# Optimization experiments

Measured on AMD Instinct MI355X. Metric: run time of the kernel, lower is better.

## Reference

```python
import jax, jax.numpy as jnp
import numpy as np
from jax import lax

OUT_PC = 64   # out_channels // 4
IN_PC = 64    # in_channels // 4
KH = KW = 3
PAD = 1
STRIDE = (1, 1)


def setup_inputs() -> dict:
    key = jax.random.key(0)
    ks = jax.random.split(key, 6)
    wshape = (OUT_PC, IN_PC, KH, KW)
    fan_in = IN_PC * KH * KW
    bound_w = float(np.sqrt(6.0 / fan_in))  # ~kaiming_uniform scale
    bound_b = 1.0 / float(np.sqrt(fan_in))
    return {
        "x": jax.random.normal(ks[0], (16, IN_PC, 64, 64, 4), dtype=jnp.float32),
        "weight_r": jax.random.uniform(ks[1], wshape, jnp.float32, -bound_w, bound_w),
        "weight_i": jax.random.uniform(ks[2], wshape, jnp.float32, -bound_w, bound_w),
        "weight_j": jax.random.uniform(ks[3], wshape, jnp.float32, -bound_w, bound_w),
        "weight_k": jax.random.uniform(ks[4], wshape, jnp.float32, -bound_w, bound_w),
        "bias_r": jax.random.uniform(ks[5], (OUT_PC,), jnp.float32, -bound_b, bound_b),
    }


def _hamilton_weight(wr, wi, wj, wk):
    # Left Hamilton-product matrix: output blocks (rows) x input blocks (cols)
    # [[ r, -i, -j, -k],
    #  [ i,  r, -k,  j],
    #  [ j,  k,  r, -i],
    #  [ k, -j,  i,  r]]
    row_r = jnp.concatenate([wr, -wi, -wj, -wk], axis=1)
    row_i = jnp.concatenate([wi,  wr, -wk,  wj], axis=1)
    row_j = jnp.concatenate([wj,  wk,  wr, -wi], axis=1)
    row_k = jnp.concatenate([wk, -wj,  wi,  wr], axis=1)
    return jnp.concatenate([row_r, row_i, row_j, row_k], axis=0)  # [4*Opc, 4*Ipc, kh, kw]


def reference(x, weight_r, weight_i, weight_j, weight_k, bias_r):
    B, C, H, W, Q = x.shape  # BCHWQ, Q == 4
    # component-major channel flatten: [B, 4*C, H, W]
    x2 = jnp.transpose(x, (0, 4, 1, 2, 3)).reshape(B, Q * C, H, W)
    w_big = _hamilton_weight(weight_r, weight_i, weight_j, weight_k)
    y = lax.conv_general_dilated(
        x2, w_big, window_strides=STRIDE,
        padding=((PAD, PAD), (PAD, PAD)),
        dimension_numbers=("NCHW", "OIHW", "NCHW"))
    Ho, Wo = y.shape[2], y.shape[3]
    opc = weight_r.shape[0]
    y = y.reshape(B, 4, opc, Ho, Wo).transpose(0, 2, 3, 4, 1)  # [B, Opc, Ho, Wo, 4]
    # bias only on the real component
    bias_full = jnp.stack(
        [bias_r, jnp.zeros_like(bias_r), jnp.zeros_like(bias_r), jnp.zeros_like(bias_r)],
        axis=-1)  # [Opc, 4]
    return y + bias_full[None, :, None, None, :]
```

## Files before the change

### kernel.cpp

```cpp
#include <hip/hip_runtime.h>

typedef __attribute__((ext_vector_type(8))) short bf16x8;
typedef __attribute__((ext_vector_type(4))) float f32x4;
typedef __attribute__((ext_vector_type(16))) float f32x16;

__device__ __forceinline__ unsigned short f2bf(float f) {
  union { float f; unsigned u; } a; a.f = f;
  unsigned u = a.u;
  u += 0x7fffu + ((u >> 16) & 1u);
  return (unsigned short)(u >> 16);
}

__global__ void prep_bt(const float* __restrict__ wr, const float* __restrict__ wi,
                        const float* __restrict__ wj, const float* __restrict__ wk,
                        unsigned short* __restrict__ btg) {
  int idx = blockIdx.x * 256 + threadIdx.x;
  if (idx >= 9 * 256 * 256) return;
  int tap = idx >> 16;
  int rem = idx & 65535;
  int n = rem >> 8, k = rem & 255;
  int opc = n >> 2, qo = n & 3, c = k >> 2, qi = k & 3;
  const int   comp[4][4] = {{0,1,2,3},{1,0,3,2},{2,3,0,1},{3,2,1,0}};
  const float sgn [4][4] = {{1.f,-1.f,-1.f,-1.f},{1.f,1.f,-1.f,1.f},
                            {1.f,1.f,1.f,-1.f},{1.f,-1.f,1.f,1.f}};
  int ci = comp[qo][qi];
  const float* wp = (ci == 0) ? wr : (ci == 1) ? wi : (ci == 2) ? wj : wk;
  float v = sgn[qo][qi] * wp[(opc * 64 + c) * 9 + tap];
  btg[idx] = f2bf(v);
}

__launch_bounds__(256, 2)
__global__ void qconv_main(const float* __restrict__ x,
                           const unsigned short* __restrict__ btg,
                           const float* __restrict__ bias,
                           float* __restrict__ out) {
  __shared__ char xwin[4 * 66 * 128];

  const int tid = threadIdx.x;
  const int nb  = (blockIdx.x & 7) * 64 + (blockIdx.x >> 3);
  const int b   = nb >> 5;
  const int h0  = (nb & 31) * 2;

  const int lane = tid & 63;
  const int wn   = tid >> 6;
  const int l31  = lane & 31;
  const int l32  = lane >> 5;

  const int w_ = tid & 63;
  if (tid < 64) {
    int hh = tid >> 4, colsel = (tid >> 3) & 1, slot = tid & 7;
    int col = colsel ? 65 : 0;
    *reinterpret_cast<f32x4*>(xwin + (hh * 66 + col) * 128 + slot * 16) =
        (f32x4){0.f, 0.f, 0.f, 0.f};
  }

  f32x16 acc[2][4];
#pragma unroll
  for (int i = 0; i < 2; ++i)
#pragma unroll
    for (int j = 0; j < 4; ++j)
      acc[i][j] = (f32x16)(0.f);

  for (int ch = 0; ch < 4; ++ch) {
    __syncthreads();

#pragma unroll
    for (int i = 0; i < 16; ++i) {
      int u  = i * 256 + tid;
      int hh = (u >> 6) & 3;
      int cl = u >> 8;
      int hp = h0 + hh - 1;
      float4 v = make_float4(0.f, 0.f, 0.f, 0.f);
      if (hp >= 0 && hp < 64)
        v = *reinterpret_cast<const float4*>(
            x + (size_t)((((b * 64 + (ch * 16 + cl)) * 64 + hp) * 64 + w_) * 4));
      unsigned lo = (unsigned)f2bf(v.x) | ((unsigned)f2bf(v.y) << 16);
      unsigned hi = (unsigned)f2bf(v.z) | ((unsigned)f2bf(v.w) << 16);
      int col  = w_ + 1;
      int byte = (hh * 66 + col) * 128 + ((cl * 8) ^ ((col & 7) << 4));
      *reinterpret_cast<uint2*>(xwin + byte) = make_uint2(lo, hi);
    }
    __syncthreads();

    const unsigned short* wb =
        btg + (size_t)(wn * 64 + l31) * 256 + ch * 64 + l32 * 8;

    bf16x8 wf[2][8];
#pragma unroll
    for (int f = 0; f < 8; ++f)
      wf[0][f] = *reinterpret_cast<const bf16x8*>(
          wb + (f & 1) * 8192 + (f >> 1) * 16);

#pragma unroll
    for (int tap = 0; tap < 9; ++tap) {
      const int cur = tap & 1;
      if (tap < 8) {
#pragma unroll
        for (int f = 0; f < 8; ++f)
          wf[cur ^ 1][f] = *reinterpret_cast<const bf16x8*>(
              wb + (tap + 1) * 65536 + (f & 1) * 8192 + (f >> 1) * 16);
      }
      const int dh = tap / 3 - 1;
      const int dw = tap % 3 - 1;
#pragma unroll
      for (int kst = 0; kst < 4; ++kst) {
        bf16x8 pf[4];
#pragma unroll
        for (int fm = 0; fm < 4; ++fm) {
          int pix = fm * 32 + l31;
          int wc  = (pix & 63) + dw + 1;
          int hh  = (pix >> 6) + dh + 1;
          int off = (hh * 66 + wc) * 128 +
                    ((kst * 32 + l32 * 16) ^ ((wc & 7) << 4));
          pf[fm] = *reinterpret_cast<const bf16x8*>(xwin + off);
        }
        __builtin_amdgcn_s_setprio(1);
#pragma unroll
        for (int fn = 0; fn < 2; ++fn)
#pragma unroll
          for (int fm = 0; fm < 4; ++fm)
            acc[fn][fm] = __builtin_amdgcn_mfma_f32_32x32x16_bf16(
                wf[cur][kst * 2 + fn], pf[fm], acc[fn][fm], 0, 0, 0);
        __builtin_amdgcn_s_setprio(0);
      }
    }
  }

#pragma unroll
  for (int fn = 0; fn < 2; ++fn) {
#pragma unroll
    for (int fm = 0; fm < 4; ++fm) {
      int pix = fm * 32 + l31;
      int w   = pix & 63;
      int h   = h0 + (pix >> 6);
#pragma unroll
      for (int g = 0; g < 4; ++g) {
        int opc = wn * 16 + fn * 8 + g * 2 + l32;
        f32x4 v = {acc[fn][fm][4 * g + 0], acc[fn][fm][4 * g + 1],
                   acc[fn][fm][4 * g + 2], acc[fn][fm][4 * g + 3]};
        v.x += bias[opc];
        *reinterpret_cast<f32x4*>(
            out + (size_t)((((b * 64 + opc) * 64 + h) * 64 + w) * 4)) = v;
      }
    }
  }
}

extern "C" void kernel_launch(void* const* d_in, const int* in_sizes, int n_in,
                              void* d_out, int out_size, void* d_ws, size_t ws_size,
                              hipStream_t stream) {
  const float* x    = (const float*)d_in[0];
  const float* wr   = (const float*)d_in[1];
  const float* wi   = (const float*)d_in[2];
  const float* wj   = (const float*)d_in[3];
  const float* wk   = (const float*)d_in[4];
  const float* bias = (const float*)d_in[5];
  unsigned short* btg = (unsigned short*)d_ws;

  prep_bt<<<2304, 256, 0, stream>>>(wr, wi, wj, wk, btg);
  qconv_main<<<512, 256, 0, stream>>>(x, btg, bias, (float*)d_out);
}
```

Baseline: 114.8 us.

## Split output channels across two blocks and retile waves to 2x2 MFMA grid

Each block now computes half of the 256 output columns for a 2-row pixel tile, and the grid doubles to 1024 blocks. Waves are arranged 2x2 over rows and channel halves with smaller accumulators, which allows a launch bound of 3 blocks per SIMD group. The LDS layout changes to a k-slot-major scheme without XOR swizzle, and weights are loaded per k-step instead of being double-buffered. The trade-off is that each input window is staged and converted twice, once per channel-half block, in exchange for higher occupancy and fewer registers.

```diff
diff --git a/kernel.cpp b/kernel.cpp
--- a/kernel.cpp
+++ b/kernel.cpp
@@ -9,6 +9,9 @@
   unsigned u = a.u;
   u += 0x7fffu + ((u >> 16) & 1u);
   return (unsigned short)(u >> 16);
+}
+__device__ __forceinline__ unsigned pk(float a, float b) {
+  return (unsigned)f2bf(a) | ((unsigned)f2bf(b) << 16);
 }
 
 __global__ void prep_bt(const float* __restrict__ wr, const float* __restrict__ wi,
@@ -29,113 +32,107 @@
   btg[idx] = f2bf(v);
 }
 
-__launch_bounds__(256, 2)
+__launch_bounds__(256, 3)
 __global__ void qconv_main(const float* __restrict__ x,
                            const unsigned short* __restrict__ btg,
                            const float* __restrict__ bias,
                            float* __restrict__ out) {
-  __shared__ char xwin[4 * 66 * 128];
+  __shared__ char xwin[4 * 8 * 66 * 16];
 
   const int tid = threadIdx.x;
-  const int nb  = (blockIdx.x & 7) * 64 + (blockIdx.x >> 3);
-  const int b   = nb >> 5;
-  const int h0  = (nb & 31) * 2;
+  const int nb  = (blockIdx.x & 7) * 128 + (blockIdx.x >> 3);
+  const int mt  = nb >> 1;
+  const int nt  = nb & 1;
+  const int b   = mt >> 5;
+  const int h0  = (mt & 31) * 2;
 
   const int lane = tid & 63;
-  const int wn   = tid >> 6;
+  const int wid  = tid >> 6;
+  const int wm   = wid & 1;
+  const int wnh  = wid >> 1;
   const int l31  = lane & 31;
   const int l32  = lane >> 5;
 
-  const int w_ = tid & 63;
+  const int w_ = lane;
+  const int sh = wid;
+
   if (tid < 64) {
-    int hh = tid >> 4, colsel = (tid >> 3) & 1, slot = tid & 7;
-    int col = colsel ? 65 : 0;
-    *reinterpret_cast<f32x4*>(xwin + (hh * 66 + col) * 128 + slot * 16) =
+    int hh = tid >> 4, ks = (tid >> 1) & 7, col = (tid & 1) ? 65 : 0;
+    *reinterpret_cast<f32x4*>(xwin + ((hh * 8 + ks) * 66 + col) * 16) =
         (f32x4){0.f, 0.f, 0.f, 0.f};
   }
 
-  f32x16 acc[2][4];
+  f32x16 acc[2][2];
 #pragma unroll
   for (int i = 0; i < 2; ++i)
 #pragma unroll
-    for (int j = 0; j < 4; ++j)
+    for (int j = 0; j < 2; ++j)
       acc[i][j] = (f32x16)(0.f);
 
   for (int ch = 0; ch < 4; ++ch) {
     __syncthreads();
 
+    const int hp = h0 + sh - 1;
+    const bool inb = (hp >= 0) && (hp < 64);
 #pragma unroll
-    for (int i = 0; i < 16; ++i) {
-      int u  = i * 256 + tid;
-      int hh = (u >> 6) & 3;
-      int cl = u >> 8;
-      int hp = h0 + hh - 1;
-      float4 v = make_float4(0.f, 0.f, 0.f, 0.f);
-      if (hp >= 0 && hp < 64)
-        v = *reinterpret_cast<const float4*>(
-            x + (size_t)((((b * 64 + (ch * 16 + cl)) * 64 + hp) * 64 + w_) * 4));
-      unsigned lo = (unsigned)f2bf(v.x) | ((unsigned)f2bf(v.y) << 16);
-      unsigned hi = (unsigned)f2bf(v.z) | ((unsigned)f2bf(v.w) << 16);
-      int col  = w_ + 1;
-      int byte = (hh * 66 + col) * 128 + ((cl * 8) ^ ((col & 7) << 4));
-      *reinterpret_cast<uint2*>(xwin + byte) = make_uint2(lo, hi);
+    for (int i = 0; i < 8; ++i) {
+      int c0 = ch * 16 + i * 2;
+      float4 v0 = make_float4(0.f, 0.f, 0.f, 0.f), v1 = v0;
+      if (inb) {
+        const float* p =
+            x + (size_t)((((b * 64 + c0) * 64 + hp) * 64 + w_) * 4);
+        v0 = *reinterpret_cast<const float4*>(p);
+        v1 = *reinterpret_cast<const float4*>(p + 16384);
+      }
+      uint4 u = make_uint4(pk(v0.x, v0.y), pk(v0.z, v0.w),
+                           pk(v1.x, v1.y), pk(v1.z, v1.w));
+      *reinterpret_cast<uint4*>(
+          xwin + ((sh * 8 + i) * 66 + (w_ + 1)) * 16) = u;
     }
     __syncthreads();
 
     const unsigned short* wb =
-        btg + (size_t)(wn * 64 + l31) * 256 + ch * 64 + l32 * 8;
-
-    bf16x8 wf[2][8];
-#pragma unroll
-    for (int f = 0; f < 8; ++f)
-      wf[0][f] = *reinterpret_cast<const bf16x8*>(
-          wb + (f & 1) * 8192 + (f >> 1) * 16);
+        btg + (size_t)(nt * 128 + wnh * 64 + l31) * 256 + ch * 64 + l32 * 8;
 
 #pragma unroll
     for (int tap = 0; tap < 9; ++tap) {
-      const int cur = tap & 1;
-      if (tap < 8) {
-#pragma unroll
-        for (int f = 0; f < 8; ++f)
-          wf[cur ^ 1][f] = *reinterpret_cast<const bf16x8*>(
-              wb + (tap + 1) * 65536 + (f & 1) * 8192 + (f >> 1) * 16);
-      }
       const int dh = tap / 3 - 1;
       const int dw = tap % 3 - 1;
+      const int hh = wm + dh + 1;
 #pragma unroll
       for (int kst = 0; kst < 4; ++kst) {
-        bf16x8 pf[4];
+        bf16x8 wf[2], pf[2];
 #pragma unroll
-        for (int fm = 0; fm < 4; ++fm) {
-          int pix = fm * 32 + l31;
-          int wc  = (pix & 63) + dw + 1;
-          int hh  = (pix >> 6) + dh + 1;
-          int off = (hh * 66 + wc) * 128 +
-                    ((kst * 32 + l32 * 16) ^ ((wc & 7) << 4));
-          pf[fm] = *reinterpret_cast<const bf16x8*>(xwin + off);
+        for (int fn = 0; fn < 2; ++fn)
+          wf[fn] = *reinterpret_cast<const bf16x8*>(
+              wb + tap * 65536 + fn * 8192 + kst * 16);
+#pragma unroll
+        for (int fm = 0; fm < 2; ++fm) {
+          int wc = fm * 32 + l31 + dw + 1;
+          pf[fm] = *reinterpret_cast<const bf16x8*>(
+              xwin + ((hh * 8 + kst * 2 + l32) * 66 + wc) * 16);
         }
         __builtin_amdgcn_s_setprio(1);
 #pragma unroll
         for (int fn = 0; fn < 2; ++fn)
 #pragma unroll
-          for (int fm = 0; fm < 4; ++fm)
+          for (int fm = 0; fm < 2; ++fm)
             acc[fn][fm] = __builtin_amdgcn_mfma_f32_32x32x16_bf16(
-                wf[cur][kst * 2 + fn], pf[fm], acc[fn][fm], 0, 0, 0);
+                wf[fn], pf[fm], acc[fn][fm], 0, 0, 0);
         __builtin_amdgcn_s_setprio(0);
       }
     }
   }
 
+  const int h = h0 + wm;
 #pragma unroll
   for (int fn = 0; fn < 2; ++fn) {
 #pragma unroll
-    for (int fm = 0; fm < 4; ++fm) {
-      int pix = fm * 32 + l31;
-      int w   = pix & 63;
-      int h   = h0 + (pix >> 6);
+    for (int fm = 0; fm < 2; ++fm) {
+      int w = fm * 32 + l31;
 #pragma unroll
       for (int g = 0; g < 4; ++g) {
-        int opc = wn * 16 + fn * 8 + g * 2 + l32;
+        int opc = nt * 32 + wnh * 16 + fn * 8 + g * 2 + l32;
         f32x4 v = {acc[fn][fm][4 * g + 0], acc[fn][fm][4 * g + 1],
                    acc[fn][fm][4 * g + 2], acc[fn][fm][4 * g + 3]};
         v.x += bias[opc];
@@ -158,5 +155,5 @@
   unsigned short* btg = (unsigned short*)d_ws;
 
   prep_bt<<<2304, 256, 0, stream>>>(wr, wi, wj, wk, btg);
-  qconv_main<<<512, 256, 0, stream>>>(x, btg, bias, (float*)d_out);
+  qconv_main<<<1024, 256, 0, stream>>>(x, btg, bias, (float*)d_out);
 }
```

New measurement: 188.7 us. +64.4%, slower.
